# Performance work log

Measured on AMD Instinct MI355X. Metric: run time of the kernel, lower is better.

The kernel has to match this reference:

```python
import jax, jax.numpy as jnp
import numpy as np

N_NODES = 10000
N_EDGES = 160000
F_IN = 128
H = 8          # heads (both layers)
C1 = 64        # conv1 per-head channels
C2 = 64        # conv2 per-head channels (= out_channels)
NEG_SLOPE = 0.2
EPS = 1e-16


def setup_inputs() -> dict:
    key = jax.random.key(0)
    ks = jax.random.split(key, 12)
    x = jax.random.normal(ks[0], (N_NODES, F_IN), dtype=jnp.float32)
    edge_index = jax.random.randint(ks[1], (2, N_EDGES), 0, N_NODES, dtype=jnp.int32)
    s = lambda fan: float(1.0 / np.sqrt(fan))
    # conv1 params
    W1 = jax.random.normal(ks[2], (F_IN, H * C1), dtype=jnp.float32) * s(F_IN)
    att_src1 = jax.random.normal(ks[3], (H, C1), dtype=jnp.float32) * s(C1)
    att_dst1 = jax.random.normal(ks[4], (H, C1), dtype=jnp.float32) * s(C1)
    bias1 = jnp.zeros((H * C1,), dtype=jnp.float32)
    t1 = jnp.ones((), dtype=jnp.float32)  # SoftmaxAggregation learnable temperature
    # conv2 params (input = H*C1 = 512)
    W2 = jax.random.normal(ks[5], (H * C1, H * C2), dtype=jnp.float32) * s(H * C1)
    att_src2 = jax.random.normal(ks[6], (H, C2), dtype=jnp.float32) * s(C2)
    att_dst2 = jax.random.normal(ks[7], (H, C2), dtype=jnp.float32) * s(C2)
    bias2 = jnp.zeros((H * C2,), dtype=jnp.float32)
    t2 = jnp.ones((), dtype=jnp.float32)
    return {"x": x, "edge_index": edge_index,
            "W1": W1, "att_src1": att_src1, "att_dst1": att_dst1, "bias1": bias1, "t1": t1,
            "W2": W2, "att_src2": att_src2, "att_dst2": att_dst2, "bias2": bias2, "t2": t2}


def _seg_softmax_weights(logits, seg, n):
    # numerically stable softmax over segments (per trailing dims)
    mx = jax.ops.segment_max(logits, seg, num_segments=n)
    mx = jnp.where(jnp.isfinite(mx), mx, 0.0)  # empty segments -> 0
    ex = jnp.exp(logits - mx[seg])
    den = jax.ops.segment_sum(ex, seg, num_segments=n)
    return ex / (den[seg] + EPS)


def gat_layer(x, src, dst, W, a_src, a_dst, bias, t, n):
    # GATConv (add_self_loops=False, concat=True) with SoftmaxAggregation(learn=True)
    h = (x @ W).reshape(n, *a_src.shape)                      # [N,H,C]
    alpha_s = jnp.sum(h * a_src, axis=-1)                     # [N,H]
    alpha_d = jnp.sum(h * a_dst, axis=-1)                     # [N,H]
    e = jax.nn.leaky_relu(alpha_s[src] + alpha_d[dst], NEG_SLOPE)  # [E,H]
    alpha = _seg_softmax_weights(e, dst, n)                   # attention softmax per dst
    m = h[src] * alpha[:, :, None]                            # [E,H,C] messages
    w = _seg_softmax_weights(t * m, dst, n)                   # learnable softmax aggregation
    out = jax.ops.segment_sum(w * m, dst, num_segments=n)     # [N,H,C]
    return out.reshape(n, -1) + bias


def reference(x, edge_index, W1, att_src1, att_dst1, bias1, t1,
              W2, att_src2, att_dst2, bias2, t2):
    src, dst = edge_index[0], edge_index[1]
    n = x.shape[0]
    h = jax.nn.relu(gat_layer(x, src, dst, W1, att_src1, att_dst1, bias1, t1, n))
    return jax.nn.relu(gat_layer(h, src, dst, W2, att_src2, att_dst2, bias2, t2, n))
```

## Files before the change

### kernel.cpp

```cpp
#include <hip/hip_runtime.h>
#include <hip/hip_bf16.h>

#define NN 10000
#define NE 160000
#define NH 8
#define NC 64
#define NF 512
#define NEG_SLOPE 0.2f
#define SEPS 1e-16f

typedef __attribute__((ext_vector_type(8))) short s8v;
typedef __attribute__((ext_vector_type(4))) float f4v;

__device__ __forceinline__ float lrelu(float x) { return x > 0.f ? x : NEG_SLOPE * x; }

__device__ __forceinline__ unsigned short bf16_rn(float f) {
  unsigned int u = __float_as_uint(f);
  return (unsigned short)((u + 0x7FFFu + ((u >> 16) & 1u)) >> 16);
}
__device__ __forceinline__ float bf16_to_f32(unsigned short h) {
  return __uint_as_float(((unsigned int)h) << 16);
}
__device__ __forceinline__ void cvt8(float4 x, float4 y, s8v& hi, s8v& lo) {
  float v[8] = {x.x, x.y, x.z, x.w, y.x, y.y, y.z, y.w};
  short h[8], l[8];
#pragma unroll
  for (int i = 0; i < 8; ++i) {
    unsigned short hb = bf16_rn(v[i]);
    h[i] = (short)hb;
    l[i] = (short)bf16_rn(v[i] - bf16_to_f32(hb));
  }
  hi = s8v{h[0], h[1], h[2], h[3], h[4], h[5], h[6], h[7]};
  lo = s8v{l[0], l[1], l[2], l[3], l[4], l[5], l[6], l[7]};
}

__global__ void zero_kernel(int* __restrict__ p, int n) {
  int i = blockIdx.x * blockDim.x + threadIdx.x;
  if (i < n) p[i] = 0;
}

__global__ void hist_kernel(const int* __restrict__ dst, int* __restrict__ counts) {
  int e = blockIdx.x * blockDim.x + threadIdx.x;
  if (e < NE) atomicAdd(&counts[dst[e]], 1);
}

__global__ __launch_bounds__(256) void scan_kernel(const int* __restrict__ counts,
                                                   int* __restrict__ row_ptr) {
  __shared__ int tmp[256];
  __shared__ int carry;
  if (threadIdx.x == 0) carry = 0;
  __syncthreads();
  for (int base = 0; base < NN; base += 256) {
    int i = base + (int)threadIdx.x;
    int v = (i < NN) ? counts[i] : 0;
    tmp[threadIdx.x] = v;
    __syncthreads();
    for (int off = 1; off < 256; off <<= 1) {
      int t = (threadIdx.x >= (unsigned)off) ? tmp[threadIdx.x - off] : 0;
      __syncthreads();
      tmp[threadIdx.x] += t;
      __syncthreads();
    }
    if (i < NN) row_ptr[i] = carry + tmp[threadIdx.x] - v;
    __syncthreads();
    if (threadIdx.x == 255) carry += tmp[255];
    __syncthreads();
  }
  if (threadIdx.x == 0) row_ptr[NN] = carry;
}

__global__ void scatter_kernel(const int* __restrict__ dst, const int* __restrict__ row_ptr,
                               int* __restrict__ cursor, int* __restrict__ sorted) {
  int e = blockIdx.x * blockDim.x + threadIdx.x;
  if (e < NE) {
    int d = dst[e];
    int r = atomicAdd(&cursor[d], 1);
    sorted[row_ptr[d] + r] = e;
  }
}

#define GBM 128
#define GBN 64
#define GBK 32

__global__ __launch_bounds__(256) void gemm_mfma(const float* __restrict__ A,
                                                 const float* __restrict__ B,
                                                 float* __restrict__ C,
                                                 int M, int K, int N) {
  __shared__ s8v smem[1536];
  unsigned short* smem_u16 = (unsigned short*)smem;
  const int tid = threadIdx.x;
  const int m0 = blockIdx.y * GBM, n0 = blockIdx.x * GBN;
  const int wid = tid >> 6, lane = tid & 63;
  const int wm = wid >> 1, wn = wid & 1;
  const int lr = lane & 15, lb = lane >> 4;

  f4v acc[4][2];
  const f4v fzero = {0.f, 0.f, 0.f, 0.f};
#pragma unroll
  for (int m = 0; m < 4; ++m)
#pragma unroll
    for (int n = 0; n < 2; ++n) acc[m][n] = fzero;

  const int arow = tid >> 1, akh = tid & 1;
  const bool avalid = (m0 + arow) < M;
  const int af = arow >> 4, ar = arow & 15;
  const int bk = (tid >> 3) * 2;
  const int bc0 = (tid & 7) * 8;
  const int bnf = bc0 >> 4, bcw = bc0 & 15;
  const int bb = bk >> 3, bi = bk & 7;

  for (int k0 = 0; k0 < K; k0 += GBK) {
    float4 a0, a1, a2, a3;
    if (avalid) {
      const float* ap = &A[(size_t)(m0 + arow) * K + k0 + akh * 16];
      a0 = *(const float4*)(ap);
      a1 = *(const float4*)(ap + 4);
      a2 = *(const float4*)(ap + 8);
      a3 = *(const float4*)(ap + 12);
    } else {
      a0 = a1 = a2 = a3 = make_float4(0.f, 0.f, 0.f, 0.f);
    }
    float4 b0, b1, b2, b3;
    if (tid < 128) {
      const float* bp = &B[(size_t)(k0 + bk) * N + n0 + bc0];
      b0 = *(const float4*)(bp);
      b1 = *(const float4*)(bp + 4);
      b2 = *(const float4*)(bp + N);
      b3 = *(const float4*)(bp + N + 4);
    }
    __syncthreads();
    {
      s8v h0, l0, h1, l1;
      cvt8(a0, a1, h0, l0);
      cvt8(a2, a3, h1, l1);
      int slot0 = (af * 4 + akh * 2 + 0) * 16 + ar;
      int slot1 = (af * 4 + akh * 2 + 1) * 16 + ar;
      smem[slot0] = h0;
      smem[slot1] = h1;
      smem[512 + slot0] = l0;
      smem[512 + slot1] = l1;
    }
    if (tid < 128) {
      float r0[8] = {b0.x, b0.y, b0.z, b0.w, b1.x, b1.y, b1.z, b1.w};
      float r1[8] = {b2.x, b2.y, b2.z, b2.w, b3.x, b3.y, b3.z, b3.w};
#pragma unroll
      for (int q = 0; q < 8; ++q) {
        unsigned short h0 = bf16_rn(r0[q]);
        unsigned short l0 = bf16_rn(r0[q] - bf16_to_f32(h0));
        unsigned short h1 = bf16_rn(r1[q]);
        unsigned short l1 = bf16_rn(r1[q] - bf16_to_f32(h1));
        int slot = (bnf * 4 + bb) * 16 + bcw + q;
        ushort2 vh = {h0, h1};
        ushort2 vl = {l0, l1};
        *(ushort2*)&smem_u16[(size_t)(1024 + slot) * 8 + bi] = vh;
        *(ushort2*)&smem_u16[(size_t)(1280 + slot) * 8 + bi] = vl;
      }
    }
    __syncthreads();
    s8v ah[4], al[4], bh[2], bl[2];
#pragma unroll
    for (int m = 0; m < 4; ++m) {
      int slot = ((wm * 4 + m) * 4 + lb) * 16 + lr;
      ah[m] = smem[slot];
      al[m] = smem[512 + slot];
    }
#pragma unroll
    for (int n = 0; n < 2; ++n) {
      int slot = ((wn * 2 + n) * 4 + lb) * 16 + lr;
      bh[n] = smem[1024 + slot];
      bl[n] = smem[1280 + slot];
    }
#pragma unroll
    for (int m = 0; m < 4; ++m)
#pragma unroll
      for (int n = 0; n < 2; ++n) {
        acc[m][n] = __builtin_amdgcn_mfma_f32_16x16x32_bf16(ah[m], bh[n], acc[m][n], 0, 0, 0);
        acc[m][n] = __builtin_amdgcn_mfma_f32_16x16x32_bf16(ah[m], bl[n], acc[m][n], 0, 0, 0);
        acc[m][n] = __builtin_amdgcn_mfma_f32_16x16x32_bf16(al[m], bh[n], acc[m][n], 0, 0, 0);
      }
  }
#pragma unroll
  for (int m = 0; m < 4; ++m) {
    int row = m0 + wm * 64 + m * 16 + lb * 4;
#pragma unroll
    for (int n = 0; n < 2; ++n) {
      int col = n0 + wn * 32 + n * 16 + lr;
#pragma unroll
      for (int j = 0; j < 4; ++j) {
        if (row + j < M) C[(size_t)(row + j) * N + col] = acc[m][n][j];
      }
    }
  }
}

__global__ __launch_bounds__(64) void att_logits_v(const float* __restrict__ h,
                                                   const float* __restrict__ att_src,
                                                   const float* __restrict__ att_dst,
                                                   float* __restrict__ as_,
                                                   float* __restrict__ ad_) {
  const int n = blockIdx.x;
  const int lane = threadIdx.x;
  const float4* hp = (const float4*)&h[(size_t)n * NF];
  float4 v0 = hp[lane * 2], v1 = hp[lane * 2 + 1];
  const int base = lane * 8;
  const float4* sp = (const float4*)&att_src[base];
  const float4* dp = (const float4*)&att_dst[base];
  float4 s0 = sp[0], s1 = sp[1], d0 = dp[0], d1 = dp[1];
  float s = v0.x * s0.x + v0.y * s0.y + v0.z * s0.z + v0.w * s0.w +
            v1.x * s1.x + v1.y * s1.y + v1.z * s1.z + v1.w * s1.w;
  float d = v0.x * d0.x + v0.y * d0.y + v0.z * d0.z + v0.w * d0.w +
            v1.x * d1.x + v1.y * d1.y + v1.z * d1.z + v1.w * d1.w;
#pragma unroll
  for (int off = 1; off <= 4; off <<= 1) {
    s += __shfl_xor(s, off);
    d += __shfl_xor(d, off);
  }
  if ((lane & 7) == 0) {
    int hd = lane >> 3;
    as_[n * NH + hd] = s;
    ad_[n * NH + hd] = d;
  }
}

__device__ __forceinline__ void online_upd(float z, float m, float& M, float& S, float& O) {
  float Mn = fmaxf(M, z);
  float a1 = __expf(M - Mn);
  float a2 = __expf(z - Mn);
  S = S * a1 + a2;
  O = O * a1 + a2 * m;
  M = Mn;
}

__global__ __launch_bounds__(256) void agg_fused(const float* __restrict__ h,
                                                 const float* __restrict__ tptr,
                                                 const int* __restrict__ src,
                                                 const int* __restrict__ sorted,
                                                 const int* __restrict__ row_ptr,
                                                 const float* __restrict__ as_,
                                                 const float* __restrict__ ad_,
                                                 const float* __restrict__ bias,
                                                 float* __restrict__ out) {
  __shared__ int s_src[256];
  __shared__ float s_x[256 * NH];
  __shared__ float s_ad[NH], s_mx[NH], s_inv[NH];
  const int n = blockIdx.x;
  const int tid = threadIdx.x;
  const int hd = tid >> 5;
  const int l32 = tid & 31;
  const int start = row_ptr[n];
  const int deg = row_ptr[n + 1] - start;
  const int c = tid * 2;
  const float t = tptr[0];

  if (tid < NH) s_ad[tid] = ad_[n * NH + tid];
  __syncthreads();

  const bool cacheable = (deg <= 256);
  float mxh = -1e30f, denh = 0.f;
  for (int base = 0; base < deg; base += 256) {
    int cnt = min(deg - base, 256);
    if (tid < cnt) s_src[tid] = src[sorted[start + base + tid]];
    __syncthreads();
    float adn = s_ad[hd];
    for (int j = l32; j < cnt; j += 32) {
      float xv = lrelu(as_[s_src[j] * NH + hd] + adn);
      if (cacheable) s_x[j * NH + hd] = xv;
      if (xv > mxh) {
        denh = denh * __expf(mxh - xv) + 1.f;
        mxh = xv;
      } else {
        denh += __expf(xv - mxh);
      }
    }
    __syncthreads();
  }
#pragma unroll
  for (int off = 16; off > 0; off >>= 1) {
    float m2 = __shfl_xor(mxh, off);
    float d2 = __shfl_xor(denh, off);
    float M = fmaxf(mxh, m2);
    denh = denh * __expf(mxh - M) + d2 * __expf(m2 - M);
    mxh = M;
  }
  if (l32 == 0) {
    s_mx[hd] = mxh;
    s_inv[hd] = 1.f / (denh + SEPS);
  }
  __syncthreads();

  float M0 = -1e30f, M1 = -1e30f, S0 = 0.f, S1 = 0.f, O0 = 0.f, O1 = 0.f;
  for (int base = 0; base < deg; base += 256) {
    int cnt = min(deg - base, 256);
    if (!cacheable) {
      __syncthreads();
      if (tid < cnt) s_src[tid] = src[sorted[start + base + tid]];
      __syncthreads();
      for (int j = l32; j < cnt; j += 32)
        s_x[j * NH + hd] = lrelu(as_[s_src[j] * NH + hd] + s_ad[hd]);
      __syncthreads();
      for (int idx = tid; idx < cnt * NH; idx += 256)
        s_x[idx] = __expf(s_x[idx] - s_mx[idx & 7]) * s_inv[idx & 7];
      __syncthreads();
    } else if (base == 0) {
      for (int idx = tid; idx < cnt * NH; idx += 256)
        s_x[idx] = __expf(s_x[idx] - s_mx[idx & 7]) * s_inv[idx & 7];
      __syncthreads();
    }
    for (int k = 0; k < cnt; ++k) {
      int sn = s_src[k];
      float a = s_x[k * NH + hd];
      float2 hv = *(const float2*)&h[(size_t)sn * NF + c];
      float m0v = hv.x * a, m1v = hv.y * a;
      online_upd(t * m0v, m0v, M0, S0, O0);
      online_upd(t * m1v, m1v, M1, S1, O1);
    }
  }
  float r0 = O0 / (S0 + SEPS) + bias[c];
  float r1 = O1 / (S1 + SEPS) + bias[c + 1];
  *(float2*)&out[(size_t)n * NF + c] = make_float2(fmaxf(r0, 0.f), fmaxf(r1, 0.f));
}

extern "C" void kernel_launch(void* const* d_in, const int* in_sizes, int n_in,
                              void* d_out, int out_size, void* d_ws, size_t ws_size,
                              hipStream_t stream) {
  const float* x     = (const float*)d_in[0];
  const int*   ei    = (const int*)d_in[1];
  const float* W1    = (const float*)d_in[2];
  const float* at_s1 = (const float*)d_in[3];
  const float* at_d1 = (const float*)d_in[4];
  const float* b1    = (const float*)d_in[5];
  const float* t1    = (const float*)d_in[6];
  const float* W2    = (const float*)d_in[7];
  const float* at_s2 = (const float*)d_in[8];
  const float* at_d2 = (const float*)d_in[9];
  const float* b2    = (const float*)d_in[10];
  const float* t2    = (const float*)d_in[11];
  float* out = (float*)d_out;

  const int* srcp = ei;
  const int* dstp = ei + NE;

  float* ws = (float*)d_ws;
  float* h_buf = ws;
  float* o_buf = h_buf + (size_t)NN * NF;
  float* asb   = o_buf + (size_t)NN * NF;
  float* adb   = asb + NN * NH;
  int* counts  = (int*)(adb + NN * NH);
  int* row_ptr = counts + NN;
  int* cursor  = row_ptr + NN + 1;
  int* sorted  = cursor + NN;

  zero_kernel<<<(NN + 255) / 256, 256, 0, stream>>>(counts, NN);
  zero_kernel<<<(NN + 255) / 256, 256, 0, stream>>>(cursor, NN);
  hist_kernel<<<(NE + 255) / 256, 256, 0, stream>>>(dstp, counts);
  scan_kernel<<<1, 256, 0, stream>>>(counts, row_ptr);
  scatter_kernel<<<(NE + 255) / 256, 256, 0, stream>>>(dstp, row_ptr, cursor, sorted);

  dim3 ggrid(NF / GBN, (NN + GBM - 1) / GBM);

  gemm_mfma<<<ggrid, 256, 0, stream>>>(x, W1, h_buf, NN, 128, NF);
  att_logits_v<<<NN, 64, 0, stream>>>(h_buf, at_s1, at_d1, asb, adb);
  agg_fused<<<NN, 256, 0, stream>>>(h_buf, t1, srcp, sorted, row_ptr, asb, adb, b1, o_buf);

  gemm_mfma<<<ggrid, 256, 0, stream>>>(o_buf, W2, h_buf, NN, NF, NF);
  att_logits_v<<<NN, 64, 0, stream>>>(h_buf, at_s2, at_d2, asb, adb);
  agg_fused<<<NN, 256, 0, stream>>>(h_buf, t2, srcp, sorted, row_ptr, asb, adb, b2, out);
}
```

Measured before the change: 320.1 us.

## Presplit GEMM operands to bf16, drop max-stabilized softmax, parallelize scan

Replaces the serial-chunk scan with a 1024-thread blocked scan. Precomputes bf16 hi/lo splits of activations and transposed weights in separate kernels so the MFMA GEMM loads ready operands instead of converting in-loop. Removes max subtraction from both segment softmaxes, using exp2 directly with plain sums, which cuts exp and compare work in aggregation but risks overflow for large logits or messages.

```diff
diff --git a/kernel.cpp b/kernel.cpp
--- a/kernel.cpp
+++ b/kernel.cpp
@@ -8,6 +8,7 @@
 #define NF 512
 #define NEG_SLOPE 0.2f
 #define SEPS 1e-16f
+#define L2E 1.44269504f
 
 typedef __attribute__((ext_vector_type(8))) short s8v;
 typedef __attribute__((ext_vector_type(4))) float f4v;
@@ -21,18 +22,6 @@
 __device__ __forceinline__ float bf16_to_f32(unsigned short h) {
   return __uint_as_float(((unsigned int)h) << 16);
 }
-__device__ __forceinline__ void cvt8(float4 x, float4 y, s8v& hi, s8v& lo) {
-  float v[8] = {x.x, x.y, x.z, x.w, y.x, y.y, y.z, y.w};
-  short h[8], l[8];
-#pragma unroll
-  for (int i = 0; i < 8; ++i) {
-    unsigned short hb = bf16_rn(v[i]);
-    h[i] = (short)hb;
-    l[i] = (short)bf16_rn(v[i] - bf16_to_f32(hb));
-  }
-  hi = s8v{h[0], h[1], h[2], h[3], h[4], h[5], h[6], h[7]};
-  lo = s8v{l[0], l[1], l[2], l[3], l[4], l[5], l[6], l[7]};
-}
 
 __global__ void zero_kernel(int* __restrict__ p, int n) {
   int i = blockIdx.x * blockDim.x + threadIdx.x;
@@ -44,29 +33,35 @@
   if (e < NE) atomicAdd(&counts[dst[e]], 1);
 }
 
-__global__ __launch_bounds__(256) void scan_kernel(const int* __restrict__ counts,
-                                                   int* __restrict__ row_ptr) {
-  __shared__ int tmp[256];
-  __shared__ int carry;
-  if (threadIdx.x == 0) carry = 0;
+__global__ __launch_bounds__(1024) void scan_fast(const int* __restrict__ counts,
+                                                  int* __restrict__ row_ptr) {
+  __shared__ int part[1024];
+  const int tid = threadIdx.x;
+  const int base = tid * 16;
+  int loc[16];
+  int s = 0;
+#pragma unroll
+  for (int i = 0; i < 16; ++i) {
+    int idx = base + i;
+    int v = (idx < NN) ? counts[idx] : 0;
+    loc[i] = s;
+    s += v;
+  }
+  part[tid] = s;
   __syncthreads();
-  for (int base = 0; base < NN; base += 256) {
-    int i = base + (int)threadIdx.x;
-    int v = (i < NN) ? counts[i] : 0;
-    tmp[threadIdx.x] = v;
-    __syncthreads();
-    for (int off = 1; off < 256; off <<= 1) {
-      int t = (threadIdx.x >= (unsigned)off) ? tmp[threadIdx.x - off] : 0;
-      __syncthreads();
-      tmp[threadIdx.x] += t;
-      __syncthreads();
-    }
-    if (i < NN) row_ptr[i] = carry + tmp[threadIdx.x] - v;
-    __syncthreads();
-    if (threadIdx.x == 255) carry += tmp[255];
-    __syncthreads();
-  }
-  if (threadIdx.x == 0) row_ptr[NN] = carry;
+  for (int off = 1; off < 1024; off <<= 1) {
+    int t = (tid >= off) ? part[tid - off] : 0;
+    __syncthreads();
+    part[tid] += t;
+    __syncthreads();
+  }
+  int pre = (tid > 0) ? part[tid - 1] : 0;
+#pragma unroll
+  for (int i = 0; i < 16; ++i) {
+    int idx = base + i;
+    if (idx < NN) row_ptr[idx] = pre + loc[i];
+  }
+  if (tid == 1023) row_ptr[NN] = part[1023];
 }
 
 __global__ void scatter_kernel(const int* __restrict__ dst, const int* __restrict__ row_ptr,
@@ -79,16 +74,59 @@
   }
 }
 
+__global__ void split_kernel(const float* __restrict__ in, unsigned short* __restrict__ hi,
+                             unsigned short* __restrict__ lo, int n4) {
+  int i = blockIdx.x * blockDim.x + threadIdx.x;
+  if (i < n4) {
+    float4 v = ((const float4*)in)[i];
+    float a[4] = {v.x, v.y, v.z, v.w};
+    ushort4 h, l;
+    unsigned short* hp = (unsigned short*)&h;
+    unsigned short* lp = (unsigned short*)&l;
+#pragma unroll
+    for (int q = 0; q < 4; ++q) {
+      unsigned short hb = bf16_rn(a[q]);
+      hp[q] = hb;
+      lp[q] = bf16_rn(a[q] - bf16_to_f32(hb));
+    }
+    ((ushort4*)hi)[i] = h;
+    ((ushort4*)lo)[i] = l;
+  }
+}
+
+__global__ __launch_bounds__(256) void tsplit_kernel(const float* __restrict__ W,
+                                                     unsigned short* __restrict__ th,
+                                                     unsigned short* __restrict__ tl,
+                                                     int K, int N) {
+  __shared__ float t[32][33];
+  const int bx = blockIdx.x * 32;
+  const int by = blockIdx.y * 32;
+  const int lx = threadIdx.x & 31, ly = threadIdx.x >> 5;
+#pragma unroll
+  for (int r = 0; r < 32; r += 8)
+    t[ly + r][lx] = W[(size_t)(by + ly + r) * N + bx + lx];
+  __syncthreads();
+#pragma unroll
+  for (int r = 0; r < 32; r += 8) {
+    float v = t[lx][ly + r];
+    unsigned short hb = bf16_rn(v);
+    size_t o = (size_t)(bx + ly + r) * K + by + lx;
+    th[o] = hb;
+    tl[o] = bf16_rn(v - bf16_to_f32(hb));
+  }
+}
+
 #define GBM 128
 #define GBN 64
 #define GBK 32
 
-__global__ __launch_bounds__(256) void gemm_mfma(const float* __restrict__ A,
-                                                 const float* __restrict__ B,
+__global__ __launch_bounds__(256) void gemm_bf16(const unsigned short* __restrict__ Ahi,
+                                                 const unsigned short* __restrict__ Alo,
+                                                 const unsigned short* __restrict__ BThi,
+                                                 const unsigned short* __restrict__ BTlo,
                                                  float* __restrict__ C,
                                                  int M, int K, int N) {
   __shared__ s8v smem[1536];
-  unsigned short* smem_u16 = (unsigned short*)smem;
   const int tid = threadIdx.x;
   const int m0 = blockIdx.y * GBM, n0 = blockIdx.x * GBN;
   const int wid = tid >> 6, lane = tid & 63;
@@ -104,59 +142,34 @@
 
   const int arow = tid >> 1, akh = tid & 1;
   const bool avalid = (m0 + arow) < M;
-  const int af = arow >> 4, ar = arow & 15;
-  const int bk = (tid >> 3) * 2;
-  const int bc0 = (tid & 7) * 8;
-  const int bnf = bc0 >> 4, bcw = bc0 & 15;
-  const int bb = bk >> 3, bi = bk & 7;
+  const int aslot = ((arow >> 4) * 4 + akh * 2) * 16 + (arow & 15);
+  const int bcol = tid >> 2, bkq = tid & 3;
+  const int bslot = ((bcol >> 4) * 4 + bkq) * 16 + (bcol & 15);
+  const s8v zv = {0, 0, 0, 0, 0, 0, 0, 0};
 
   for (int k0 = 0; k0 < K; k0 += GBK) {
-    float4 a0, a1, a2, a3;
+    s8v a_h0 = zv, a_h1 = zv, a_l0 = zv, a_l1 = zv, b_h, b_l;
     if (avalid) {
-      const float* ap = &A[(size_t)(m0 + arow) * K + k0 + akh * 16];
-      a0 = *(const float4*)(ap);
-      a1 = *(const float4*)(ap + 4);
-      a2 = *(const float4*)(ap + 8);
-      a3 = *(const float4*)(ap + 12);
-    } else {
-      a0 = a1 = a2 = a3 = make_float4(0.f, 0.f, 0.f, 0.f);
-    }
-    float4 b0, b1, b2, b3;
-    if (tid < 128) {
-      const float* bp = &B[(size_t)(k0 + bk) * N + n0 + bc0];
-      b0 = *(const float4*)(bp);
-      b1 = *(const float4*)(bp + 4);
-      b2 = *(const float4*)(bp + N);
-      b3 = *(const float4*)(bp + N + 4);
-    }
-    __syncthreads();
+      const unsigned short* ap = &Ahi[(size_t)(m0 + arow) * K + k0 + akh * 16];
+      const unsigned short* alp = &Alo[(size_t)(m0 + arow) * K + k0 + akh * 16];
+      a_h0 = *(const s8v*)ap;
+      a_h1 = *(const s8v*)(ap + 8);
+      a_l0 = *(const s8v*)alp;
+      a_l1 = *(const s8v*)(alp + 8);
+    }
     {
-      s8v h0, l0, h1, l1;
-      cvt8(a0, a1, h0, l0);
-      cvt8(a2, a3, h1, l1);
-      int slot0 = (af * 4 + akh * 2 + 0) * 16 + ar;
-      int slot1 = (af * 4 + akh * 2 + 1) * 16 + ar;
-      smem[slot0] = h0;
-      smem[slot1] = h1;
-      smem[512 + slot0] = l0;
-      smem[512 + slot1] = l1;
-    }
-    if (tid < 128) {
-      float r0[8] = {b0.x, b0.y, b0.z, b0.w, b1.x, b1.y, b1.z, b1.w};
-      float r1[8] = {b2.x, b2.y, b2.z, b2.w, b3.x, b3.y, b3.z, b3.w};
-#pragma unroll
-      for (int q = 0; q < 8; ++q) {
-        unsigned short h0 = bf16_rn(r0[q]);
-        unsigned short l0 = bf16_rn(r0[q] - bf16_to_f32(h0));
-        unsigned short h1 = bf16_rn(r1[q]);
-        unsigned short l1 = bf16_rn(r1[q] - bf16_to_f32(h1));
-        int slot = (bnf * 4 + bb) * 16 + bcw + q;
-        ushort2 vh = {h0, h1};
-        ushort2 vl = {l0, l1};
-        *(ushort2*)&smem_u16[(size_t)(1024 + slot) * 8 + bi] = vh;
-        *(ushort2*)&smem_u16[(size_t)(1280 + slot) * 8 + bi] = vl;
-      }
-    }
+      const unsigned short* bp = &BThi[(size_t)(n0 + bcol) * K + k0 + bkq * 8];
+      const unsigned short* blp = &BTlo[(size_t)(n0 + bcol) * K + k0 + bkq * 8];
+      b_h = *(const s8v*)bp;
+      b_l = *(const s8v*)blp;
+    }
+    __syncthreads();
+    smem[aslot] = a_h0;
+    smem[aslot + 16] = a_h1;
+    smem[512 + aslot] = a_l0;
+    smem[512 + aslot + 16] = a_l1;
+    smem[1024 + bslot] = b_h;
+    smem[1280 + bslot] = b_l;
     __syncthreads();
     s8v ah[4], al[4], bh[2], bl[2];
 #pragma unroll
@@ -223,15 +236,6 @@
   }
 }
 
-__device__ __forceinline__ void online_upd(float z, float m, float& M, float& S, float& O) {
-  float Mn = fmaxf(M, z);
-  float a1 = __expf(M - Mn);
-  float a2 = __expf(z - Mn);
-  S = S * a1 + a2;
-  O = O * a1 + a2 * m;
-  M = Mn;
-}
-
 __global__ __launch_bounds__(256) void agg_fused(const float* __restrict__ h,
                                                  const float* __restrict__ tptr,
                                                  const int* __restrict__ src,
@@ -243,7 +247,7 @@
                                                  float* __restrict__ out) {
   __shared__ int s_src[256];
   __shared__ float s_x[256 * NH];
-  __shared__ float s_ad[NH], s_mx[NH], s_inv[NH];
+  __shared__ float s_ad[NH], s_inv[NH];
   const int n = blockIdx.x;
   const int tid = threadIdx.x;
   const int hd = tid >> 5;
@@ -251,69 +255,65 @@
   const int start = row_ptr[n];
   const int deg = row_ptr[n + 1] - start;
   const int c = tid * 2;
-  const float t = tptr[0];
+  const float tl2 = tptr[0] * L2E;
 
   if (tid < NH) s_ad[tid] = ad_[n * NH + tid];
   __syncthreads();
 
   const bool cacheable = (deg <= 256);
-  float mxh = -1e30f, denh = 0.f;
+  float denh = 0.f;
   for (int base = 0; base < deg; base += 256) {
     int cnt = min(deg - base, 256);
     if (tid < cnt) s_src[tid] = src[sorted[start + base + tid]];
     __syncthreads();
     float adn = s_ad[hd];
     for (int j = l32; j < cnt; j += 32) {
-      float xv = lrelu(as_[s_src[j] * NH + hd] + adn);
-      if (cacheable) s_x[j * NH + hd] = xv;
-      if (xv > mxh) {
-        denh = denh * __expf(mxh - xv) + 1.f;
-        mxh = xv;
-      } else {
-        denh += __expf(xv - mxh);
-      }
-    }
-    __syncthreads();
-  }
-#pragma unroll
-  for (int off = 16; off > 0; off >>= 1) {
-    float m2 = __shfl_xor(mxh, off);
-    float d2 = __shfl_xor(denh, off);
-    float M = fmaxf(mxh, m2);
-    denh = denh * __expf(mxh - M) + d2 * __expf(m2 - M);
-    mxh = M;
-  }
-  if (l32 == 0) {
-    s_mx[hd] = mxh;
-    s_inv[hd] = 1.f / (denh + SEPS);
-  }
+      float e = __builtin_exp2f(L2E * lrelu(as_[s_src[j] * NH + hd] + adn));
+      if (cacheable) s_x[j * NH + hd] = e;
+      denh += e;
+    }
+    __syncthreads();
+  }
+#pragma unroll
+  for (int off = 16; off > 0; off >>= 1) denh += __shfl_xor(denh, off);
+  if (l32 == 0) s_inv[hd] = 1.f / (denh + SEPS);
   __syncthreads();
 
-  float M0 = -1e30f, M1 = -1e30f, S0 = 0.f, S1 = 0.f, O0 = 0.f, O1 = 0.f;
-  for (int base = 0; base < deg; base += 256) {
-    int cnt = min(deg - base, 256);
-    if (!cacheable) {
+  float S0 = 0.f, S1 = 0.f, O0 = 0.f, O1 = 0.f;
+  if (cacheable) {
+    for (int idx = tid; idx < deg * NH; idx += 256) s_x[idx] *= s_inv[idx & 7];
+    __syncthreads();
+#pragma unroll 4
+    for (int k = 0; k < deg; ++k) {
+      int sn = s_src[k];
+      float a = s_x[k * NH + hd];
+      float2 hv = *(const float2*)&h[(size_t)sn * NF + c];
+      float m0 = hv.x * a, m1 = hv.y * a;
+      float e0 = __builtin_exp2f(tl2 * m0);
+      float e1 = __builtin_exp2f(tl2 * m1);
+      S0 += e0; O0 += e0 * m0;
+      S1 += e1; O1 += e1 * m1;
+    }
+  } else {
+    for (int base = 0; base < deg; base += 256) {
+      int cnt = min(deg - base, 256);
       __syncthreads();
       if (tid < cnt) s_src[tid] = src[sorted[start + base + tid]];
       __syncthreads();
       for (int j = l32; j < cnt; j += 32)
-        s_x[j * NH + hd] = lrelu(as_[s_src[j] * NH + hd] + s_ad[hd]);
+        s_x[j * NH + hd] =
+            __builtin_exp2f(L2E * lrelu(as_[s_src[j] * NH + hd] + s_ad[hd])) * s_inv[hd];
       __syncthreads();
-      for (int idx = tid; idx < cnt * NH; idx += 256)
-        s_x[idx] = __expf(s_x[idx] - s_mx[idx & 7]) * s_inv[idx & 7];
-      __syncthreads();
-    } else if (base == 0) {
-      for (int idx = tid; idx < cnt * NH; idx += 256)
-        s_x[idx] = __expf(s_x[idx] - s_mx[idx & 7]) * s_inv[idx & 7];
-      __syncthreads();
-    }
-    for (int k = 0; k < cnt; ++k) {
-      int sn = s_src[k];
-      float a = s_x[k * NH + hd];
-      float2 hv = *(const float2*)&h[(size_t)sn * NF + c];
-      float m0v = hv.x * a, m1v = hv.y * a;
-      online_upd(t * m0v, m0v, M0, S0, O0);
-      online_upd(t * m1v, m1v, M1, S1, O1);
+      for (int k = 0; k < cnt; ++k) {
+        int sn = s_src[k];
+        float a = s_x[k * NH + hd];
+        float2 hv = *(const float2*)&h[(size_t)sn * NF + c];
+        float m0 = hv.x * a, m1 = hv.y * a;
+        float e0 = __builtin_exp2f(tl2 * m0);
+        float e1 = __builtin_exp2f(tl2 * m1);
+        S0 += e0; O0 += e0 * m0;
+        S1 += e1; O1 += e1 * m1;
+      }
     }
   }
   float r0 = O0 / (S0 + SEPS) + bias[c];
@@ -346,24 +346,38 @@
   float* o_buf = h_buf + (size_t)NN * NF;
   float* asb   = o_buf + (size_t)NN * NF;
   float* adb   = asb + NN * NH;
-  int* counts  = (int*)(adb + NN * NH);
+  unsigned short* xs_hi = (unsigned short*)(adb + NN * NH);
+  unsigned short* xs_lo = xs_hi + (size_t)NN * 128;
+  unsigned short* wt1h  = xs_lo + (size_t)NN * 128;
+  unsigned short* wt1l  = wt1h + 512 * 128;
+  unsigned short* wt2h  = wt1l + 512 * 128;
+  unsigned short* wt2l  = wt2h + 512 * 512;
+  int* counts  = (int*)(wt2l + 512 * 512);
   int* row_ptr = counts + NN;
   int* cursor  = row_ptr + NN + 1;
   int* sorted  = cursor + NN;
+  unsigned short* y1h = (unsigned short*)h_buf;
+  unsigned short* y1l = y1h + (size_t)NN * NF;
 
   zero_kernel<<<(NN + 255) / 256, 256, 0, stream>>>(counts, NN);
   zero_kernel<<<(NN + 255) / 256, 256, 0, stream>>>(cursor, NN);
   hist_kernel<<<(NE + 255) / 256, 256, 0, stream>>>(dstp, counts);
-  scan_kernel<<<1, 256, 0, stream>>>(counts, row_ptr);
+  scan_fast<<<1, 1024, 0, stream>>>(counts, row_ptr);
   scatter_kernel<<<(NE + 255) / 256, 256, 0, stream>>>(dstp, row_ptr, cursor, sorted);
 
+  split_kernel<<<(NN * 128 / 4 + 255) / 256, 256, 0, stream>>>(x, xs_hi, xs_lo, NN * 128 / 4);
+  tsplit_kernel<<<dim3(512 / 32, 128 / 32), 256, 0, stream>>>(W1, wt1h, wt1l, 128, 512);
+  tsplit_kernel<<<dim3(512 / 32, 512 / 32), 256, 0, stream>>>(W2, wt2h, wt2l, 512, 512);
+
   dim3 ggrid(NF / GBN, (NN + GBM - 1) / GBM);
 
-  gemm_mfma<<<ggrid, 256, 0, stream>>>(x, W1, h_buf, NN, 128, NF);
+  gemm_bf16<<<ggrid, 256, 0, stream>>>(xs_hi, xs_lo, wt1h, wt1l, h_buf, NN, 128, NF);
   att_logits_v<<<NN, 64, 0, stream>>>(h_buf, at_s1, at_d1, asb, adb);
   agg_fused<<<NN, 256, 0, stream>>>(h_buf, t1, srcp, sorted, row_ptr, asb, adb, b1, o_buf);
 
-  gemm_mfma<<<ggrid, 256, 0, stream>>>(o_buf, W2, h_buf, NN, NF, NF);
-  att_logits_v<<<NN, 64, 0, stream>>>(h_buf, at_s2, at_d2, asb, adb);
-  agg_fused<<<NN, 256, 0, stream>>>(h_buf, t2, srcp, sorted, row_ptr, asb, adb, b2, out);
-}
+  split_kernel<<<((size_t)NN * NF / 4 + 255) / 256, 256, 0, stream>>>(o_buf, y1h, y1l,
+                                                                      NN * NF / 4);
+  gemm_bf16<<<ggrid, 256, 0, stream>>>(y1h, y1l, wt2h, wt2l, o_buf, NN, NF, NF);
+  att_logits_v<<<NN, 64, 0, stream>>>(o_buf, at_s2, at_d2, asb, adb);
+  agg_fused<<<NN, 256, 0, stream>>>(o_buf, t2, srcp, sorted, row_ptr, asb, adb, b2, out);
+}
```

Result: faster. 289.7 us (-9.5%).
